# Kernel optimization log

Measured on AMD Instinct MI355X. Metric: run time of the kernel, lower is better.

Reference implementation:

```python
import jax, jax.numpy as jnp
import numpy as np

N_NODES = 50000
N_EDGES = 800000
D = 128


def setup_inputs() -> dict:
    key = jax.random.key(0)
    k1, k2, k3, k4 = jax.random.split(key, 4)
    x1 = jax.random.normal(k1, (N_NODES, D), dtype=jnp.float32)
    adj = jax.random.randint(k2, (2, N_EDGES), 0, N_NODES, dtype=jnp.int64)
    scale = 1.0 / np.sqrt(D)
    W1 = jax.random.normal(k3, (D, D), dtype=jnp.float32) * scale
    b1 = jnp.zeros((D,), dtype=jnp.float32)
    W2 = jax.random.normal(k4, (D, D), dtype=jnp.float32) * scale
    b2 = jnp.zeros((D,), dtype=jnp.float32)
    return {"x1": x1, "adj": adj, "W1": W1, "b1": b1, "W2": W2, "b2": b2}


def reference(x1, adj, W1, b1, W2, b2):
    num_nodes = x1.shape[0]
    # message: gather source-node features per edge -> [E, D]
    edge_x = x1[adj[0]]
    # aggregate: scatter-max into destination nodes -> [N, D]
    x2 = jax.ops.segment_max(edge_x, adj[1], num_segments=num_nodes)
    # empty segments yield -inf; torch_scatter fills them with 0
    x2 = jnp.where(jnp.isneginf(x2), jnp.zeros_like(x2), x2)
    # combine: residual add + 2-layer MLP
    h = jax.nn.relu((x1 + x2) @ W1 + b1)
    return h @ W2 + b2
```

## Files before the change

kernel.cpp:

```cpp
#include <hip/hip_runtime.h>
#include <stdint.h>
#include <math.h>

#define DD 128
#define ROWS 128
#define CAP 64

typedef unsigned short u16;
typedef unsigned int   u32;
typedef __attribute__((ext_vector_type(8))) short bf16x8;
typedef __attribute__((ext_vector_type(4))) float f32x4;

__device__ __forceinline__ u16 f2bf(float f) {
    u32 u = __float_as_uint(f);
    return (u16)((u + 0x7fffu + ((u >> 16) & 1u)) >> 16);
}
__device__ __forceinline__ float bf_lo(u32 u) { return __uint_as_float(u << 16); }
__device__ __forceinline__ float bf_hi(u32 u) { return __uint_as_float(u & 0xffff0000u); }

__device__ __forceinline__ int swz(int row, int byte_in_row) {
    return row * 256 + (byte_in_row ^ ((row & 7) << 4));
}

__global__ __launch_bounds__(256) void fill_cvt_w_k(
    const int* __restrict__ adj, int* __restrict__ deg,
    u16* __restrict__ ent,
    const float* __restrict__ x1, u16* __restrict__ x1bf,
    const float* __restrict__ W1, const float* __restrict__ W2,
    u16* __restrict__ W1T, u16* __restrict__ W2T,
    int n_edges, int n_nodes)
{
    if ((int)blockIdx.x == (int)gridDim.x - 1) {
        for (int t = threadIdx.x; t < 4096; t += 256) {
            int m = t >> 11;
            int idx = t & 2047;
            int c = idx >> 4, k8 = idx & 15;
            const float* W = m ? W2 : W1;
            u16* WT = m ? W2T : W1T;
            u16 tmp[8];
            #pragma unroll
            for (int j = 0; j < 8; ++j) tmp[j] = f2bf(W[(k8 * 8 + j) * DD + c]);
            uint4 v;
            v.x = (u32)tmp[0] | ((u32)tmp[1] << 16);
            v.y = (u32)tmp[2] | ((u32)tmp[3] << 16);
            v.z = (u32)tmp[4] | ((u32)tmp[5] << 16);
            v.w = (u32)tmp[6] | ((u32)tmp[7] << 16);
            *(uint4*)((char*)WT + swz(c, k8 * 16)) = v;
        }
        return;
    }
    int t = blockIdx.x * 256 + threadIdx.x;

    if (t < n_edges) {
        int src = adj[t];
        int dst = adj[n_edges + t];
        if ((unsigned)src < (unsigned)n_nodes && (unsigned)dst < (unsigned)n_nodes) {
            int slot = atomicAdd(&deg[dst], 1);
            if (slot < CAP) ent[(size_t)dst * CAP + slot] = (u16)src;
        }
    }

    int n_cvt = n_nodes * 16;
    if (t < n_cvt) {
        const float4* x4 = (const float4*)x1;
        float4 a = x4[(size_t)t * 2];
        float4 b = x4[(size_t)t * 2 + 1];
        uint4 v;
        v.x = (u32)f2bf(a.x) | ((u32)f2bf(a.y) << 16);
        v.y = (u32)f2bf(a.z) | ((u32)f2bf(a.w) << 16);
        v.z = (u32)f2bf(b.x) | ((u32)f2bf(b.y) << 16);
        v.w = (u32)f2bf(b.z) | ((u32)f2bf(b.w) << 16);
        ((uint4*)x1bf)[t] = v;
    }
}

__global__ __launch_bounds__(256) void gather_max_k(
    const u16* __restrict__ x1bf, const int* __restrict__ deg,
    const u16* __restrict__ ent, u16* __restrict__ xin, int n_nodes)
{
    int node = blockIdx.x * 16 + (threadIdx.x >> 4);
    int q = threadIdx.x & 15;
    if (node >= n_nodes) return;
    int d = deg[node];
    if (d > CAP) d = CAP;
    const u16* en = ent + (size_t)node * CAP;
    const uint4* xb = (const uint4*)x1bf;

    float m[4][8];
    #pragma unroll
    for (int j = 0; j < 4; ++j)
        #pragma unroll
        for (int k = 0; k < 8; ++k) m[j][k] = -INFINITY;

    int i = 0;
    for (; i + 3 < d; i += 4) {
        uint2 e4 = *(const uint2*)(en + i);
        int s0 = e4.x & 0xffff, s1 = e4.x >> 16;
        int s2 = e4.y & 0xffff, s3 = e4.y >> 16;
        uint4 v0 = xb[(size_t)s0 * 16 + q];
        uint4 v1 = xb[(size_t)s1 * 16 + q];
        uint4 v2 = xb[(size_t)s2 * 16 + q];
        uint4 v3 = xb[(size_t)s3 * 16 + q];
        #define ACC(J, V) \
            m[J][0]=fmaxf(m[J][0],bf_lo(V.x)); m[J][1]=fmaxf(m[J][1],bf_hi(V.x)); \
            m[J][2]=fmaxf(m[J][2],bf_lo(V.y)); m[J][3]=fmaxf(m[J][3],bf_hi(V.y)); \
            m[J][4]=fmaxf(m[J][4],bf_lo(V.z)); m[J][5]=fmaxf(m[J][5],bf_hi(V.z)); \
            m[J][6]=fmaxf(m[J][6],bf_lo(V.w)); m[J][7]=fmaxf(m[J][7],bf_hi(V.w));
        ACC(0, v0) ACC(1, v1) ACC(2, v2) ACC(3, v3)
    }
    for (; i < d; ++i) {
        int s0 = en[i];
        uint4 v0 = xb[(size_t)s0 * 16 + q];
        ACC(0, v0)
        #undef ACC
    }
    #pragma unroll
    for (int k = 0; k < 8; ++k)
        m[0][k] = fmaxf(fmaxf(m[0][k], m[1][k]), fmaxf(m[2][k], m[3][k]));

    uint4 sv = xb[(size_t)node * 16 + q];
    float r[8];
    r[0]=bf_lo(sv.x); r[1]=bf_hi(sv.x); r[2]=bf_lo(sv.y); r[3]=bf_hi(sv.y);
    r[4]=bf_lo(sv.z); r[5]=bf_hi(sv.z); r[6]=bf_lo(sv.w); r[7]=bf_hi(sv.w);
    if (d > 0) {
        #pragma unroll
        for (int k = 0; k < 8; ++k) r[k] += m[0][k];
    }
    uint4 o;
    o.x = (u32)f2bf(r[0]) | ((u32)f2bf(r[1]) << 16);
    o.y = (u32)f2bf(r[2]) | ((u32)f2bf(r[3]) << 16);
    o.z = (u32)f2bf(r[4]) | ((u32)f2bf(r[5]) << 16);
    o.w = (u32)f2bf(r[6]) | ((u32)f2bf(r[7]) << 16);
    ((uint4*)xin)[(size_t)node * 16 + q] = o;
}

__global__ __launch_bounds__(256, 2) void mlp_mfma_k(
    const u16* __restrict__ xin,
    const u16* __restrict__ W1T, const float* __restrict__ b1,
    const u16* __restrict__ W2T, const float* __restrict__ b2,
    float* __restrict__ out, int n_rows)
{
    __shared__ uint4 sXq[ROWS * 16];
    __shared__ uint4 sWq[128 * 16];
    char* sX = (char*)sXq;
    char* sW = (char*)sWq;

    const int tid  = threadIdx.x;
    const int wave = tid >> 6;
    const int lane = tid & 63;
    const int lhi  = lane >> 4, llo = lane & 15;
    const int row0 = blockIdx.x * ROWS;

    {
        const uint4* src = (const uint4*)xin;
        #pragma unroll
        for (int i = tid; i < ROWS * 16; i += 256) {
            int r = i >> 4, c8 = i & 15;
            uint4 v = make_uint4(0, 0, 0, 0);
            if (row0 + r < n_rows) v = src[(size_t)(row0 + r) * 16 + c8];
            *(uint4*)(sX + swz(r, c8 * 16)) = v;
        }
        const uint4* wsrc = (const uint4*)W1T;
        #pragma unroll
        for (int i = tid; i < 2048; i += 256) sWq[i] = wsrc[i];
    }
    __syncthreads();

    const int wrow0 = wave * 32;

    f32x4 acc[2][8];
    #pragma unroll
    for (int mi = 0; mi < 2; ++mi)
        #pragma unroll
        for (int nj = 0; nj < 8; ++nj)
            acc[mi][nj] = (f32x4){0.f, 0.f, 0.f, 0.f};

    #pragma unroll
    for (int kstep = 0; kstep < 4; ++kstep) {
        int kb = (kstep * 32 + lhi * 8) * 2;
        int ra = wrow0 + llo, rb = wrow0 + 16 + llo;
        bf16x8 a0 = *(const bf16x8*)(sX + swz(ra, kb));
        bf16x8 a1 = *(const bf16x8*)(sX + swz(rb, kb));
        #pragma unroll
        for (int nj = 0; nj < 8; ++nj) {
            int c = nj * 16 + llo;
            bf16x8 b = *(const bf16x8*)(sW + swz(c, kb));
            acc[0][nj] = __builtin_amdgcn_mfma_f32_16x16x32_bf16(a0, b, acc[0][nj], 0, 0, 0);
            acc[1][nj] = __builtin_amdgcn_mfma_f32_16x16x32_bf16(a1, b, acc[1][nj], 0, 0, 0);
        }
    }

    #pragma unroll
    for (int nj = 0; nj < 8; ++nj) {
        int col = nj * 16 + llo;
        float bv = b1[col];
        #pragma unroll
        for (int mi = 0; mi < 2; ++mi) {
            #pragma unroll
            for (int r = 0; r < 4; ++r) {
                int row = wrow0 + mi * 16 + lhi * 4 + r;
                float h = fmaxf(acc[mi][nj][r] + bv, 0.f);
                *(u16*)(sX + swz(row, col * 2)) = f2bf(h);
            }
        }
    }
    __syncthreads();

    {
        const uint4* wsrc = (const uint4*)W2T;
        #pragma unroll
        for (int i = tid; i < 2048; i += 256) sWq[i] = wsrc[i];
    }
    __syncthreads();

    #pragma unroll
    for (int mi = 0; mi < 2; ++mi)
        #pragma unroll
        for (int nj = 0; nj < 8; ++nj)
            acc[mi][nj] = (f32x4){0.f, 0.f, 0.f, 0.f};

    #pragma unroll
    for (int kstep = 0; kstep < 4; ++kstep) {
        int kb = (kstep * 32 + lhi * 8) * 2;
        int ra = wrow0 + llo, rb = wrow0 + 16 + llo;
        bf16x8 a0 = *(const bf16x8*)(sX + swz(ra, kb));
        bf16x8 a1 = *(const bf16x8*)(sX + swz(rb, kb));
        #pragma unroll
        for (int nj = 0; nj < 8; ++nj) {
            int c = nj * 16 + llo;
            bf16x8 b = *(const bf16x8*)(sW + swz(c, kb));
            acc[0][nj] = __builtin_amdgcn_mfma_f32_16x16x32_bf16(a0, b, acc[0][nj], 0, 0, 0);
            acc[1][nj] = __builtin_amdgcn_mfma_f32_16x16x32_bf16(a1, b, acc[1][nj], 0, 0, 0);
        }
    }

    #pragma unroll
    for (int nj = 0; nj < 8; ++nj) {
        int col = nj * 16 + llo;
        float bv = b2[col];
        #pragma unroll
        for (int mi = 0; mi < 2; ++mi) {
            #pragma unroll
            for (int r = 0; r < 4; ++r) {
                int row = row0 + wrow0 + mi * 16 + lhi * 4 + r;
                if (row < n_rows)
                    out[(size_t)row * DD + col] = acc[mi][nj][r] + bv;
            }
        }
    }
}

extern "C" void kernel_launch(void* const* d_in, const int* in_sizes, int n_in,
                              void* d_out, int out_size, void* d_ws, size_t ws_size,
                              hipStream_t stream) {
    const float* x1  = (const float*)d_in[0];
    const int*   adj = (const int*)d_in[1];
    const float* W1  = (const float*)d_in[2];
    const float* b1  = (const float*)d_in[3];
    const float* W2  = (const float*)d_in[4];
    const float* b2  = (const float*)d_in[5];
    float* out = (float*)d_out;

    const int n_nodes = in_sizes[0] / DD;
    const int n_edges = in_sizes[1] / 2;

    u16* x1bf = (u16*)d_out;

    char* ws = (char*)d_ws;
    size_t off = 0;
    u16* xin = (u16*)(ws + off); off += (size_t)n_nodes * DD * sizeof(u16);
    u16* ent = (u16*)(ws + off); off += (size_t)n_nodes * CAP * sizeof(u16);
    u16* W1T = (u16*)(ws + off); off += (size_t)DD * DD * sizeof(u16);
    u16* W2T = (u16*)(ws + off); off += (size_t)DD * DD * sizeof(u16);
    int* deg = (int*)(ws + off); off += (size_t)n_nodes * sizeof(int);

    hipMemsetAsync(deg, 0, (size_t)n_nodes * sizeof(int), stream);

    int eb = (n_edges + 255) / 256;
    fill_cvt_w_k<<<eb + 1, 256, 0, stream>>>(adj, deg, ent, x1, x1bf,
                                             W1, W2, W1T, W2T, n_edges, n_nodes);

    gather_max_k<<<(n_nodes + 15) / 16, 256, 0, stream>>>(x1bf, deg, ent, xin, n_nodes);
    mlp_mfma_k<<<(n_nodes + ROWS - 1) / ROWS, 256, 0, stream>>>(
        xin, W1T, b1, W2T, b2, out, n_nodes);
}
```

Measured before the change: 120.2 us.

## Fuse gather-max aggregation into MLP kernel, staging bf16 rows in LDS

```diff
diff --git a/kernel.cpp b/kernel.cpp
--- a/kernel.cpp
+++ b/kernel.cpp
@@ -3,7 +3,7 @@
 #include <math.h>
 
 #define DD 128
-#define ROWS 128
+#define ROWS 64
 #define CAP 64
 
 typedef unsigned short u16;
@@ -23,8 +23,7 @@
 }
 
 __global__ __launch_bounds__(256) void fill_cvt_w_k(
-    const int* __restrict__ adj, int* __restrict__ deg,
-    u16* __restrict__ ent,
+    const int* __restrict__ adj, int* __restrict__ deg, u16* __restrict__ ent,
     const float* __restrict__ x1, u16* __restrict__ x1bf,
     const float* __restrict__ W1, const float* __restrict__ W2,
     u16* __restrict__ W1T, u16* __restrict__ W2T,
@@ -74,68 +73,9 @@
     }
 }
 
-__global__ __launch_bounds__(256) void gather_max_k(
+__global__ __launch_bounds__(256, 3) void gather_mlp_k(
     const u16* __restrict__ x1bf, const int* __restrict__ deg,
-    const u16* __restrict__ ent, u16* __restrict__ xin, int n_nodes)
-{
-    int node = blockIdx.x * 16 + (threadIdx.x >> 4);
-    int q = threadIdx.x & 15;
-    if (node >= n_nodes) return;
-    int d = deg[node];
-    if (d > CAP) d = CAP;
-    const u16* en = ent + (size_t)node * CAP;
-    const uint4* xb = (const uint4*)x1bf;
-
-    float m[4][8];
-    #pragma unroll
-    for (int j = 0; j < 4; ++j)
-        #pragma unroll
-        for (int k = 0; k < 8; ++k) m[j][k] = -INFINITY;
-
-    int i = 0;
-    for (; i + 3 < d; i += 4) {
-        uint2 e4 = *(const uint2*)(en + i);
-        int s0 = e4.x & 0xffff, s1 = e4.x >> 16;
-        int s2 = e4.y & 0xffff, s3 = e4.y >> 16;
-        uint4 v0 = xb[(size_t)s0 * 16 + q];
-        uint4 v1 = xb[(size_t)s1 * 16 + q];
-        uint4 v2 = xb[(size_t)s2 * 16 + q];
-        uint4 v3 = xb[(size_t)s3 * 16 + q];
-        #define ACC(J, V) \
-            m[J][0]=fmaxf(m[J][0],bf_lo(V.x)); m[J][1]=fmaxf(m[J][1],bf_hi(V.x)); \
-            m[J][2]=fmaxf(m[J][2],bf_lo(V.y)); m[J][3]=fmaxf(m[J][3],bf_hi(V.y)); \
-            m[J][4]=fmaxf(m[J][4],bf_lo(V.z)); m[J][5]=fmaxf(m[J][5],bf_hi(V.z)); \
-            m[J][6]=fmaxf(m[J][6],bf_lo(V.w)); m[J][7]=fmaxf(m[J][7],bf_hi(V.w));
-        ACC(0, v0) ACC(1, v1) ACC(2, v2) ACC(3, v3)
-    }
-    for (; i < d; ++i) {
-        int s0 = en[i];
-        uint4 v0 = xb[(size_t)s0 * 16 + q];
-        ACC(0, v0)
-        #undef ACC
-    }
-    #pragma unroll
-    for (int k = 0; k < 8; ++k)
-        m[0][k] = fmaxf(fmaxf(m[0][k], m[1][k]), fmaxf(m[2][k], m[3][k]));
-
-    uint4 sv = xb[(size_t)node * 16 + q];
-    float r[8];
-    r[0]=bf_lo(sv.x); r[1]=bf_hi(sv.x); r[2]=bf_lo(sv.y); r[3]=bf_hi(sv.y);
-    r[4]=bf_lo(sv.z); r[5]=bf_hi(sv.z); r[6]=bf_lo(sv.w); r[7]=bf_hi(sv.w);
-    if (d > 0) {
-        #pragma unroll
-        for (int k = 0; k < 8; ++k) r[k] += m[0][k];
-    }
-    uint4 o;
-    o.x = (u32)f2bf(r[0]) | ((u32)f2bf(r[1]) << 16);
-    o.y = (u32)f2bf(r[2]) | ((u32)f2bf(r[3]) << 16);
-    o.z = (u32)f2bf(r[4]) | ((u32)f2bf(r[5]) << 16);
-    o.w = (u32)f2bf(r[6]) | ((u32)f2bf(r[7]) << 16);
-    ((uint4*)xin)[(size_t)node * 16 + q] = o;
-}
-
-__global__ __launch_bounds__(256, 2) void mlp_mfma_k(
-    const u16* __restrict__ xin,
+    const u16* __restrict__ ent,
     const u16* __restrict__ W1T, const float* __restrict__ b1,
     const u16* __restrict__ W2T, const float* __restrict__ b2,
     float* __restrict__ out, int n_rows)
@@ -152,41 +92,87 @@
     const int row0 = blockIdx.x * ROWS;
 
     {
-        const uint4* src = (const uint4*)xin;
-        #pragma unroll
-        for (int i = tid; i < ROWS * 16; i += 256) {
-            int r = i >> 4, c8 = i & 15;
-            uint4 v = make_uint4(0, 0, 0, 0);
-            if (row0 + r < n_rows) v = src[(size_t)(row0 + r) * 16 + c8];
-            *(uint4*)(sX + swz(r, c8 * 16)) = v;
-        }
         const uint4* wsrc = (const uint4*)W1T;
         #pragma unroll
         for (int i = tid; i < 2048; i += 256) sWq[i] = wsrc[i];
     }
+
+    const uint4* xb = (const uint4*)x1bf;
+    const int q = tid & 15;
+    #pragma unroll
+    for (int pass = 0; pass < 4; ++pass) {
+        int l = pass * 16 + (tid >> 4);
+        int node = row0 + l;
+        uint4 o = make_uint4(0, 0, 0, 0);
+        if (node < n_rows) {
+            int d = deg[node];
+            if (d > CAP) d = CAP;
+            const u16* en = ent + (size_t)node * CAP;
+
+            float m[4][8];
+            #pragma unroll
+            for (int j = 0; j < 4; ++j)
+                #pragma unroll
+                for (int k = 0; k < 8; ++k) m[j][k] = -INFINITY;
+
+            int i = 0;
+            for (; i + 3 < d; i += 4) {
+                uint2 e4 = *(const uint2*)(en + i);
+                int s0 = e4.x & 0xffff, s1 = e4.x >> 16;
+                int s2 = e4.y & 0xffff, s3 = e4.y >> 16;
+                uint4 v0 = xb[(size_t)s0 * 16 + q];
+                uint4 v1 = xb[(size_t)s1 * 16 + q];
+                uint4 v2 = xb[(size_t)s2 * 16 + q];
+                uint4 v3 = xb[(size_t)s3 * 16 + q];
+                #define ACC(J, V) \
+                    m[J][0]=fmaxf(m[J][0],bf_lo(V.x)); m[J][1]=fmaxf(m[J][1],bf_hi(V.x)); \
+                    m[J][2]=fmaxf(m[J][2],bf_lo(V.y)); m[J][3]=fmaxf(m[J][3],bf_hi(V.y)); \
+                    m[J][4]=fmaxf(m[J][4],bf_lo(V.z)); m[J][5]=fmaxf(m[J][5],bf_hi(V.z)); \
+                    m[J][6]=fmaxf(m[J][6],bf_lo(V.w)); m[J][7]=fmaxf(m[J][7],bf_hi(V.w));
+                ACC(0, v0) ACC(1, v1) ACC(2, v2) ACC(3, v3)
+            }
+            for (; i < d; ++i) {
+                int s0 = en[i];
+                uint4 v0 = xb[(size_t)s0 * 16 + q];
+                ACC(0, v0)
+                #undef ACC
+            }
+            #pragma unroll
+            for (int k = 0; k < 8; ++k)
+                m[0][k] = fmaxf(fmaxf(m[0][k], m[1][k]), fmaxf(m[2][k], m[3][k]));
+
+            uint4 sv = xb[(size_t)node * 16 + q];
+            float r[8];
+            r[0]=bf_lo(sv.x); r[1]=bf_hi(sv.x); r[2]=bf_lo(sv.y); r[3]=bf_hi(sv.y);
+            r[4]=bf_lo(sv.z); r[5]=bf_hi(sv.z); r[6]=bf_lo(sv.w); r[7]=bf_hi(sv.w);
+            if (d > 0) {
+                #pragma unroll
+                for (int k = 0; k < 8; ++k) r[k] += m[0][k];
+            }
+            o.x = (u32)f2bf(r[0]) | ((u32)f2bf(r[1]) << 16);
+            o.y = (u32)f2bf(r[2]) | ((u32)f2bf(r[3]) << 16);
+            o.z = (u32)f2bf(r[4]) | ((u32)f2bf(r[5]) << 16);
+            o.w = (u32)f2bf(r[6]) | ((u32)f2bf(r[7]) << 16);
+        }
+        *(uint4*)(sX + swz(l, q * 16)) = o;
+    }
     __syncthreads();
 
-    const int wrow0 = wave * 32;
-
-    f32x4 acc[2][8];
-    #pragma unroll
-    for (int mi = 0; mi < 2; ++mi)
-        #pragma unroll
-        for (int nj = 0; nj < 8; ++nj)
-            acc[mi][nj] = (f32x4){0.f, 0.f, 0.f, 0.f};
+    const int wrow0 = wave * 16;
+
+    f32x4 acc[8];
+    #pragma unroll
+    for (int nj = 0; nj < 8; ++nj) acc[nj] = (f32x4){0.f, 0.f, 0.f, 0.f};
 
     #pragma unroll
     for (int kstep = 0; kstep < 4; ++kstep) {
         int kb = (kstep * 32 + lhi * 8) * 2;
-        int ra = wrow0 + llo, rb = wrow0 + 16 + llo;
-        bf16x8 a0 = *(const bf16x8*)(sX + swz(ra, kb));
-        bf16x8 a1 = *(const bf16x8*)(sX + swz(rb, kb));
+        bf16x8 a0 = *(const bf16x8*)(sX + swz(wrow0 + llo, kb));
         #pragma unroll
         for (int nj = 0; nj < 8; ++nj) {
             int c = nj * 16 + llo;
             bf16x8 b = *(const bf16x8*)(sW + swz(c, kb));
-            acc[0][nj] = __builtin_amdgcn_mfma_f32_16x16x32_bf16(a0, b, acc[0][nj], 0, 0, 0);
-            acc[1][nj] = __builtin_amdgcn_mfma_f32_16x16x32_bf16(a1, b, acc[1][nj], 0, 0, 0);
+            acc[nj] = __builtin_amdgcn_mfma_f32_16x16x32_bf16(a0, b, acc[nj], 0, 0, 0);
         }
     }
 
@@ -195,13 +181,10 @@
         int col = nj * 16 + llo;
         float bv = b1[col];
         #pragma unroll
-        for (int mi = 0; mi < 2; ++mi) {
-            #pragma unroll
-            for (int r = 0; r < 4; ++r) {
-                int row = wrow0 + mi * 16 + lhi * 4 + r;
-                float h = fmaxf(acc[mi][nj][r] + bv, 0.f);
-                *(u16*)(sX + swz(row, col * 2)) = f2bf(h);
-            }
+        for (int r = 0; r < 4; ++r) {
+            int row = wrow0 + lhi * 4 + r;
+            float h = fmaxf(acc[nj][r] + bv, 0.f);
+            *(u16*)(sX + swz(row, col * 2)) = f2bf(h);
         }
     }
     __syncthreads();
@@ -214,23 +197,17 @@
     __syncthreads();
 
     #pragma unroll
-    for (int mi = 0; mi < 2; ++mi)
-        #pragma unroll
-        for (int nj = 0; nj < 8; ++nj)
-            acc[mi][nj] = (f32x4){0.f, 0.f, 0.f, 0.f};
+    for (int nj = 0; nj < 8; ++nj) acc[nj] = (f32x4){0.f, 0.f, 0.f, 0.f};
 
     #pragma unroll
     for (int kstep = 0; kstep < 4; ++kstep) {
         int kb = (kstep * 32 + lhi * 8) * 2;
-        int ra = wrow0 + llo, rb = wrow0 + 16 + llo;
-        bf16x8 a0 = *(const bf16x8*)(sX + swz(ra, kb));
-        bf16x8 a1 = *(const bf16x8*)(sX + swz(rb, kb));
+        bf16x8 a0 = *(const bf16x8*)(sX + swz(wrow0 + llo, kb));
         #pragma unroll
         for (int nj = 0; nj < 8; ++nj) {
             int c = nj * 16 + llo;
             bf16x8 b = *(const bf16x8*)(sW + swz(c, kb));
-            acc[0][nj] = __builtin_amdgcn_mfma_f32_16x16x32_bf16(a0, b, acc[0][nj], 0, 0, 0);
-            acc[1][nj] = __builtin_amdgcn_mfma_f32_16x16x32_bf16(a1, b, acc[1][nj], 0, 0, 0);
+            acc[nj] = __builtin_amdgcn_mfma_f32_16x16x32_bf16(a0, b, acc[nj], 0, 0, 0);
         }
     }
 
@@ -239,13 +216,10 @@
         int col = nj * 16 + llo;
         float bv = b2[col];
         #pragma unroll
-        for (int mi = 0; mi < 2; ++mi) {
-            #pragma unroll
-            for (int r = 0; r < 4; ++r) {
-                int row = row0 + wrow0 + mi * 16 + lhi * 4 + r;
-                if (row < n_rows)
-                    out[(size_t)row * DD + col] = acc[mi][nj][r] + bv;
-            }
+        for (int r = 0; r < 4; ++r) {
+            int row = row0 + wrow0 + lhi * 4 + r;
+            if (row < n_rows)
+                out[(size_t)row * DD + col] = acc[nj][r] + bv;
         }
     }
 }
@@ -264,15 +238,13 @@
     const int n_nodes = in_sizes[0] / DD;
     const int n_edges = in_sizes[1] / 2;
 
-    u16* x1bf = (u16*)d_out;
-
     char* ws = (char*)d_ws;
     size_t off = 0;
-    u16* xin = (u16*)(ws + off); off += (size_t)n_nodes * DD * sizeof(u16);
-    u16* ent = (u16*)(ws + off); off += (size_t)n_nodes * CAP * sizeof(u16);
-    u16* W1T = (u16*)(ws + off); off += (size_t)DD * DD * sizeof(u16);
-    u16* W2T = (u16*)(ws + off); off += (size_t)DD * DD * sizeof(u16);
-    int* deg = (int*)(ws + off); off += (size_t)n_nodes * sizeof(int);
+    u16* x1bf = (u16*)(ws + off); off += (size_t)n_nodes * DD * sizeof(u16);
+    u16* ent  = (u16*)(ws + off); off += (size_t)n_nodes * CAP * sizeof(u16);
+    u16* W1T  = (u16*)(ws + off); off += (size_t)DD * DD * sizeof(u16);
+    u16* W2T  = (u16*)(ws + off); off += (size_t)DD * DD * sizeof(u16);
+    int* deg  = (int*)(ws + off); off += (size_t)n_nodes * sizeof(int);
 
     hipMemsetAsync(deg, 0, (size_t)n_nodes * sizeof(int), stream);
 
@@ -280,7 +252,6 @@
     fill_cvt_w_k<<<eb + 1, 256, 0, stream>>>(adj, deg, ent, x1, x1bf,
                                              W1, W2, W1T, W2T, n_edges, n_nodes);
 
-    gather_max_k<<<(n_nodes + 15) / 16, 256, 0, stream>>>(x1bf, deg, ent, xin, n_nodes);
-    mlp_mfma_k<<<(n_nodes + ROWS - 1) / ROWS, 256, 0, stream>>>(
-        xin, W1T, b1, W2T, b2, out, n_nodes);
-}
+    gather_mlp_k<<<(n_nodes + ROWS - 1) / ROWS, 256, 0, stream>>>(
+        x1bf, deg, ent, W1T, b1, W2T, b2, out, n_nodes);
+}
```

Result: slower. 135.8 us (+12.9%).
